# Optimization experiments

Measured on AMD Instinct MI355X. Metric: run time of the kernel, lower is better.

The kernel has to match this reference:

```python
import jax, jax.numpy as jnp
from jax import lax
import numpy as np

EPS = 1e-3  # Keras BatchNormalization default epsilon

def cond_conv(x, experts, rw, rb):
    # x: [B,H,W,Cin]; experts: [E,kh,kw,Cin,Cout]
    pooled = jnp.mean(x, axis=(1, 2))                       # [B,Cin]
    route = jax.nn.sigmoid(pooled @ rw + rb)                # [B,E]
    kernels = jnp.einsum('be,ehwio->bhwio', route, experts) # per-example kernel
    def conv1(xi, ki):
        return lax.conv_general_dilated(
            xi[None], ki, window_strides=(1, 1), padding='SAME',
            dimension_numbers=('NHWC', 'HWIO', 'NHWC'))[0]
    return jax.vmap(conv1)(x, kernels)

def bn_inf(x, gamma, beta, mean, var):
    inv = gamma * lax.rsqrt(var + EPS)
    return x * inv + (beta - mean * inv)

def maxpool2(x):
    return lax.reduce_window(x, -jnp.inf, lax.max,
                             (1, 2, 2, 1), (1, 2, 2, 1), 'SAME')

def se_block(x, w1, w2):
    s = jnp.mean(x, axis=(1, 2))          # [B,C]
    s = jax.nn.relu(s @ w1)
    s = jax.nn.sigmoid(s @ w2)
    return x * s[:, None, None, :]

def setup_inputs() -> dict:
    key = jax.random.key(0)
    ks = jax.random.split(key, 12)
    d = {
        'x': jax.random.normal(ks[0], (64, 128, 128, 6), jnp.float32),
        'experts1': jax.random.normal(ks[1], (3, 3, 3, 6, 32), jnp.float32) * 0.1,
        'route1_w': jax.random.normal(ks[2], (6, 3), jnp.float32) * 0.1,
        'route1_b': jnp.zeros((3,), jnp.float32),
        'bn1_gamma': jnp.ones((32,), jnp.float32), 'bn1_beta': jnp.zeros((32,), jnp.float32),
        'bn1_mean': jnp.zeros((32,), jnp.float32), 'bn1_var': jnp.ones((32,), jnp.float32),
        'se1_w1': jax.random.normal(ks[3], (32, 2), jnp.float32) * 0.1,
        'se1_w2': jax.random.normal(ks[4], (2, 32), jnp.float32) * 0.1,
        'experts2': jax.random.normal(ks[5], (3, 3, 3, 32, 64), jnp.float32) * 0.05,
        'route2_w': jax.random.normal(ks[6], (32, 3), jnp.float32) * 0.1,
        'route2_b': jnp.zeros((3,), jnp.float32),
        'bn2_gamma': jnp.ones((64,), jnp.float32), 'bn2_beta': jnp.zeros((64,), jnp.float32),
        'bn2_mean': jnp.zeros((64,), jnp.float32), 'bn2_var': jnp.ones((64,), jnp.float32),
        'se2_w1': jax.random.normal(ks[7], (64, 4), jnp.float32) * 0.1,
        'se2_w2': jax.random.normal(ks[8], (4, 64), jnp.float32) * 0.1,
        'experts3': jax.random.normal(ks[9], (3, 3, 3, 64, 128), jnp.float32) * 0.05,
        'route3_w': jax.random.normal(ks[10], (64, 3), jnp.float32) * 0.1,
        'route3_b': jnp.zeros((3,), jnp.float32),
        'bn3_gamma': jnp.ones((128,), jnp.float32), 'bn3_beta': jnp.zeros((128,), jnp.float32),
        'bn3_mean': jnp.zeros((128,), jnp.float32), 'bn3_var': jnp.ones((128,), jnp.float32),
    }
    return d

def reference(x, experts1, route1_w, route1_b, bn1_gamma, bn1_beta, bn1_mean, bn1_var,
              se1_w1, se1_w2, experts2, route2_w, route2_b, bn2_gamma, bn2_beta,
              bn2_mean, bn2_var, se2_w1, se2_w2, experts3, route3_w, route3_b,
              bn3_gamma, bn3_beta, bn3_mean, bn3_var):
    h = cond_conv(x, experts1, route1_w, route1_b)
    h = jax.nn.relu(bn_inf(h, bn1_gamma, bn1_beta, bn1_mean, bn1_var))
    h = maxpool2(h)                       # [B,64,64,32]
    h = se_block(h, se1_w1, se1_w2)
    h = cond_conv(h, experts2, route2_w, route2_b)
    h = jax.nn.relu(bn_inf(h, bn2_gamma, bn2_beta, bn2_mean, bn2_var))
    h = maxpool2(h)                       # [B,32,32,64]
    h = se_block(h, se2_w1, se2_w2)
    h = cond_conv(h, experts3, route3_w, route3_b)
    h = bn_inf(h, bn3_gamma, bn3_beta, bn3_mean, bn3_var)
    return jnp.mean(h, axis=(1, 2))       # [B,128]
```

## Files before the change

kernel.cpp:

```cpp
#include <hip/hip_runtime.h>

#define EPSBN 1e-3f

typedef unsigned short ushort_t;
typedef __attribute__((ext_vector_type(8))) short bf8;
typedef __attribute__((ext_vector_type(4))) float f4;

__device__ __forceinline__ float sigmoidf_(float z) {
  return 1.0f / (1.0f + expf(-z));
}

__device__ __forceinline__ ushort_t f2bf(float x) {
  union { float f; unsigned u; } v; v.f = x;
  unsigned r = (v.u + 0x7fffu + ((v.u >> 16) & 1u)) >> 16;
  return (ushort_t)r;
}

__global__ void k_mean_x(const float* __restrict__ x, float* __restrict__ part) {
  const int b = blockIdx.x >> 2;
  const int q = blockIdx.x & 3;
  const int tid = threadIdx.x;
  float acc[6] = {0.f, 0.f, 0.f, 0.f, 0.f, 0.f};
  const float* xb = x + (size_t)b * 98304 + (size_t)q * 24576;
  for (int p = 0; p < 4; ++p) {
    const float* base = xb + (size_t)p * 6144 + (size_t)tid * 24;
#pragma unroll
    for (int k = 0; k < 6; ++k) {
      const float4 v = *(const float4*)(base + k * 4);
      acc[(4 * k + 0) % 6] += v.x;
      acc[(4 * k + 1) % 6] += v.y;
      acc[(4 * k + 2) % 6] += v.z;
      acc[(4 * k + 3) % 6] += v.w;
    }
  }
#pragma unroll
  for (int c = 0; c < 6; ++c)
    for (int off = 32; off > 0; off >>= 1) acc[c] += __shfl_down(acc[c], off, 64);
  __shared__ float red[4][6];
  const int lane = tid & 63, w = tid >> 6;
  if (lane == 0) {
#pragma unroll
    for (int c = 0; c < 6; ++c) red[w][c] = acc[c];
  }
  __syncthreads();
  if (tid < 6) {
    part[blockIdx.x * 6 + tid] = red[0][tid] + red[1][tid] + red[2][tid] + red[3][tid];
  }
}

__global__ __launch_bounds__(256)
void k_conv1(const float* __restrict__ x, const float* __restrict__ meanx_part,
             const float* __restrict__ experts1,
             const float* __restrict__ rw, const float* __restrict__ rbias,
             const float* __restrict__ gamma, const float* __restrict__ beta,
             const float* __restrict__ bnmean, const float* __restrict__ bnvar,
             ushort_t* __restrict__ p1b, float* __restrict__ part_m1) {
  const int bid = blockIdx.x;
  const int b = bid >> 3;
  const int tyi = (bid >> 1) & 3;
  const int txi = bid & 1;
  __shared__ __align__(16) ushort_t patch[34 * 68 * 8];
  __shared__ float route_s[3];
  __shared__ float mred[4][32];
  const int tid = threadIdx.x;
  const float* xb = x + (size_t)b * (128 * 128 * 6);

  if (tid < 3) {
    float z = rbias[tid];
    for (int c = 0; c < 6; ++c) {
      const float s = meanx_part[(b * 4 + 0) * 6 + c] + meanx_part[(b * 4 + 1) * 6 + c] +
                      meanx_part[(b * 4 + 2) * 6 + c] + meanx_part[(b * 4 + 3) * 6 + c];
      z += (s * (1.0f / 16384.0f)) * rw[c * 3 + tid];
    }
    route_s[tid] = sigmoidf_(z);
  }

  for (int v = tid; v < 34 * 68; v += 256) {
    const int ry = v / 68, p = v - ry * 68;
    const int gy = tyi * 32 - 1 + ry, gx = txi * 64 - 1 + p;
    uint4 u = make_uint4(0u, 0u, 0u, 0u);
    if (((unsigned)gy < 128u) && ((unsigned)gx < 128u)) {
      const float* s = xb + ((size_t)(gy * 128 + gx)) * 6;
      const float2 a0 = *(const float2*)s;
      const float2 a1 = *(const float2*)(s + 2);
      const float2 a2 = *(const float2*)(s + 4);
      u.x = (unsigned)f2bf(a0.x) | ((unsigned)f2bf(a0.y) << 16);
      u.y = (unsigned)f2bf(a1.x) | ((unsigned)f2bf(a1.y) << 16);
      u.z = (unsigned)f2bf(a2.x) | ((unsigned)f2bf(a2.y) << 16);
      u.w = 0u;
    }
    *(uint4*)(patch + (size_t)v * 8) = u;
  }
  __syncthreads();

  const int w = tid >> 6;
  const int lane = tid & 63;
  const int lx = lane & 15, lg = lane >> 4;

  const float r0 = route_s[0], r1 = route_s[1], r2 = route_s[2];
  const int co0 = lx, co1 = 16 + lx;
  const float inv0 = gamma[co0] * rsqrtf(bnvar[co0] + EPSBN);
  const float bias0 = beta[co0] - bnmean[co0] * inv0;
  const float inv1 = gamma[co1] * rsqrtf(bnvar[co1] + EPSBN);
  const float bias1 = beta[co1] - bnmean[co1] * inv1;

  bf8 Bf[3][2];
#pragma unroll
  for (int ky = 0; ky < 3; ++ky) {
#pragma unroll
    for (int nt = 0; nt < 2; ++nt) {
      const int co = nt * 16 + lx;
      const float inv = nt ? inv1 : inv0;
#pragma unroll
      for (int j = 0; j < 8; ++j) {
        float val = 0.f;
        if (j < 6 && lg < 3) {
          const int idx = ((ky * 3 + lg) * 6 + j) * 32 + co;
          val = (r0 * experts1[idx] + r1 * experts1[1728 + idx] +
                 r2 * experts1[3456 + idx]) * inv;
        }
        Bf[ky][nt][j] = (short)f2bf(val);
      }
    }
  }

  float msum0 = 0.f, msum1 = 0.f;

#pragma unroll
  for (int xt = 0; xt < 4; ++xt) {
    bf8 Af[10];
#pragma unroll
    for (int r = 0; r < 10; ++r)
      Af[r] = *(const bf8*)(patch + ((size_t)(w * 8 + r) * 68 + xt * 16 + lx + lg) * 8);
#pragma unroll
    for (int rp = 0; rp < 4; ++rp) {
      const int prow = tyi * 16 + w * 4 + rp;
      f4 acc0[2], acc1[2];
#pragma unroll
      for (int nt = 0; nt < 2; ++nt) {
        acc0[nt] = (f4){0.f, 0.f, 0.f, 0.f};
        acc1[nt] = (f4){0.f, 0.f, 0.f, 0.f};
      }
#pragma unroll
      for (int ky = 0; ky < 3; ++ky) {
#pragma unroll
        for (int nt = 0; nt < 2; ++nt) {
          acc0[nt] = __builtin_amdgcn_mfma_f32_16x16x32_bf16(Af[rp * 2 + ky], Bf[ky][nt], acc0[nt], 0, 0, 0);
          acc1[nt] = __builtin_amdgcn_mfma_f32_16x16x32_bf16(Af[rp * 2 + ky + 1], Bf[ky][nt], acc1[nt], 0, 0, 0);
        }
      }
#pragma unroll
      for (int nt = 0; nt < 2; ++nt) {
        const float bias = nt ? bias1 : bias0;
        const int co = nt * 16 + lx;
#pragma unroll
        for (int q = 0; q < 2; ++q) {
          const float m0 = fmaxf(acc0[nt][2 * q] + bias, 0.f);
          const float m1 = fmaxf(acc0[nt][2 * q + 1] + bias, 0.f);
          const float m2 = fmaxf(acc1[nt][2 * q] + bias, 0.f);
          const float m3 = fmaxf(acc1[nt][2 * q + 1] + bias, 0.f);
          const float mx = fmaxf(fmaxf(m0, m1), fmaxf(m2, m3));
          if (nt) msum1 += mx; else msum0 += mx;
          const int pcol = txi * 32 + xt * 8 + lg * 2 + q;
          p1b[(((size_t)b * 64 + prow) * 64 + pcol) * 32 + co] = f2bf(mx);
        }
      }
    }
  }

  msum0 += __shfl_xor(msum0, 16, 64);
  msum0 += __shfl_xor(msum0, 32, 64);
  msum1 += __shfl_xor(msum1, 16, 64);
  msum1 += __shfl_xor(msum1, 32, 64);
  if (lg == 0) {
    mred[w][lx] = msum0;
    mred[w][16 + lx] = msum1;
  }
  __syncthreads();
  if (tid < 32) {
    part_m1[(size_t)bid * 32 + tid] =
        mred[0][tid] + mred[1][tid] + mred[2][tid] + mred[3][tid];
  }
}

__global__ void k_buildk2(const float* __restrict__ part_m1,
                          const float* __restrict__ experts2,
                          const float* __restrict__ rw, const float* __restrict__ rb,
                          const float* __restrict__ w1, const float* __restrict__ w2,
                          const float* __restrict__ gamma, const float* __restrict__ var,
                          ushort_t* __restrict__ k2pb) {
  const int b = blockIdx.x / 3;
  const int seg = blockIdx.x - b * 3;
  const int tid = threadIdx.x;
  __shared__ float m1[32], h[2], s1[32], route[3];
  if (tid < 32) {
    float s = 0.f;
#pragma unroll
    for (int k = 0; k < 8; ++k) s += part_m1[(size_t)(b * 8 + k) * 32 + tid];
    m1[tid] = s * (1.0f / 4096.0f);
  }
  __syncthreads();
  if (tid < 2) {
    float z = 0.f;
    for (int c = 0; c < 32; ++c) z += m1[c] * w1[c * 2 + tid];
    h[tid] = fmaxf(z, 0.f);
  }
  __syncthreads();
  if (tid < 32) s1[tid] = sigmoidf_(h[0] * w2[tid] + h[1] * w2[32 + tid]);
  __syncthreads();
  if (tid < 3) {
    float z = rb[tid];
    for (int c = 0; c < 32; ++c) z += m1[c] * s1[c] * rw[c * 3 + tid];
    route[tid] = sigmoidf_(z);
  }
  __syncthreads();
  const float r0 = route[0], r1 = route[1], r2 = route[2];
  const int t_lo = seg * 6144, t_hi = t_lo + 6144;
  for (int t = t_lo + tid; t < t_hi; t += 256) {
    const int co = t & 63;
    const int ci = (t >> 6) & 31;
    const int tap = t >> 11;
    const float inv = gamma[co] * rsqrtf(var[co] + EPSBN);
    const float v = r0 * experts2[t] + r1 * experts2[18432 + t] + r2 * experts2[2 * 18432 + t];
    k2pb[(size_t)b * 18432 + ((size_t)tap * 64 + co) * 32 + ci] = f2bf(v * s1[ci] * inv);
  }
}

__global__ __launch_bounds__(256)
void k_conv2(const ushort_t* __restrict__ p1b, const ushort_t* __restrict__ k2pb,
             const float* __restrict__ gamma, const float* __restrict__ beta,
             const float* __restrict__ bnmean, const float* __restrict__ bnvar,
             float* __restrict__ part_s3) {
  const int bi = blockIdx.x;
  const int b = bi >> 5;
  const int tile = (bi >> 1) & 15;
  const int cog = bi & 1;
  const int ty = tile >> 2, tx = tile & 3;
  __shared__ __align__(16) short smem[24480];
  short* As = smem;
  short* Bs = smem + 12960;
  const int tid = threadIdx.x;

  const ushort_t* pb = p1b + (size_t)b * 131072;
  for (int v = tid; v < 1296; v += 256) {
    const int cell = v >> 2, part = v & 3;
    const int ly = cell / 18, lx2 = cell - ly * 18;
    const int gy = ty * 16 - 1 + ly, gx = tx * 16 - 1 + lx2;
    uint4 d = make_uint4(0u, 0u, 0u, 0u);
    if (((unsigned)gy < 64u) && ((unsigned)gx < 64u))
      d = *(const uint4*)(pb + (((size_t)gy << 6) + gx) * 32 + part * 8);
    *(uint4*)(As + (ly * 18 + lx2) * 40 + part * 8) = d;
  }
  for (int v = tid; v < 1152; v += 256) {
    const int r = v >> 2, part = v & 3;
    const int t = r >> 5, n = r & 31;
    const uint4 d = *(const uint4*)(k2pb + (size_t)b * 18432 +
                                    ((size_t)(t * 64 + cog * 32 + n)) * 32 + part * 8);
    *(uint4*)(Bs + r * 40 + part * 8) = d;
  }
  __syncthreads();

  const int w = tid >> 6;
  const int lane = tid & 63;
  const int lx = lane & 15, lg = lane >> 4;

  f4 acc[4][2];
#pragma unroll
  for (int mt = 0; mt < 4; ++mt)
#pragma unroll
    for (int nt = 0; nt < 2; ++nt)
      acc[mt][nt] = (f4){0.f, 0.f, 0.f, 0.f};

#pragma unroll
  for (int kx = 0; kx < 3; ++kx) {
    bf8 Af[6];
#pragma unroll
    for (int r = 0; r < 6; ++r)
      Af[r] = *(const bf8*)(As + ((4 * w + r) * 18 + lx + kx) * 40 + (lg << 3));
#pragma unroll
    for (int ky = 0; ky < 3; ++ky) {
      const int t = ky * 3 + kx;
      const bf8 Bf0 = *(const bf8*)(Bs + ((t << 5) + lx) * 40 + (lg << 3));
      const bf8 Bf1 = *(const bf8*)(Bs + ((t << 5) + 16 + lx) * 40 + (lg << 3));
#pragma unroll
      for (int mt = 0; mt < 4; ++mt) {
        acc[mt][0] = __builtin_amdgcn_mfma_f32_16x16x32_bf16(Af[ky + mt], Bf0, acc[mt][0], 0, 0, 0);
        acc[mt][1] = __builtin_amdgcn_mfma_f32_16x16x32_bf16(Af[ky + mt], Bf1, acc[mt][1], 0, 0, 0);
      }
    }
  }

  float inv[2], bias[2];
#pragma unroll
  for (int nt = 0; nt < 2; ++nt) {
    const int co = cog * 32 + nt * 16 + lx;
    inv[nt] = gamma[co] * rsqrtf(bnvar[co] + EPSBN);
    bias[nt] = beta[co] - bnmean[co] * inv[nt];
  }
  float agg[2][9];
#pragma unroll
  for (int nt = 0; nt < 2; ++nt)
#pragma unroll
    for (int a = 0; a < 9; ++a) agg[nt][a] = 0.f;

#pragma unroll
  for (int half = 0; half < 2; ++half) {
    const int prow = ty * 8 + 2 * w + half;
    const bool rT = (prow == 0), rB = (prow == 31);
#pragma unroll
    for (int q = 0; q < 2; ++q) {
      const int pcol = tx * 8 + 2 * lg + q;
      const bool cL = (pcol == 0), cR = (pcol == 31);
#pragma unroll
      for (int nt = 0; nt < 2; ++nt) {
        const float m0 = fmaxf(acc[2 * half][nt][2 * q] + bias[nt], 0.f);
        const float m1 = fmaxf(acc[2 * half][nt][2 * q + 1] + bias[nt], 0.f);
        const float m2 = fmaxf(acc[2 * half + 1][nt][2 * q] + bias[nt], 0.f);
        const float m3 = fmaxf(acc[2 * half + 1][nt][2 * q + 1] + bias[nt], 0.f);
        const float mx = fmaxf(fmaxf(m0, m1), fmaxf(m2, m3));
        agg[nt][0] += mx;
        if (rT) agg[nt][1] += mx;
        if (rB) agg[nt][2] += mx;
        if (cL) agg[nt][3] += mx;
        if (cR) agg[nt][4] += mx;
        if (rT && cL) agg[nt][5] += mx;
        if (rT && cR) agg[nt][6] += mx;
        if (rB && cL) agg[nt][7] += mx;
        if (rB && cR) agg[nt][8] += mx;
      }
    }
  }

#pragma unroll
  for (int nt = 0; nt < 2; ++nt)
#pragma unroll
    for (int a = 0; a < 9; ++a) {
      float v = agg[nt][a];
      v += __shfl_xor(v, 16, 64);
      v += __shfl_xor(v, 32, 64);
      agg[nt][a] = v;
    }
  __syncthreads();
  float* sred = (float*)smem;
  if (lg == 0) {
#pragma unroll
    for (int nt = 0; nt < 2; ++nt)
#pragma unroll
      for (int a = 0; a < 9; ++a)
        sred[((w * 2 + nt) * 16 + lx) * 9 + a] = agg[nt][a];
  }
  __syncthreads();
  for (int v = tid; v < 288; v += 256) {
    const int a = v >> 5;
    const int colocal = v & 31;
    const int nt = colocal >> 4, lxx = colocal & 15;
    float s = 0.f;
#pragma unroll
    for (int ww = 0; ww < 4; ++ww) s += sred[((ww * 2 + nt) * 16 + lxx) * 9 + a];
    part_s3[(size_t)bi * 288 + v] = s;
  }
}

__global__ __launch_bounds__(512)
void k_final(const float* __restrict__ part_s3, const float* __restrict__ experts3,
             const float* __restrict__ rw, const float* __restrict__ rb,
             const float* __restrict__ w1, const float* __restrict__ w2,
             const float* __restrict__ gamma, const float* __restrict__ beta,
             const float* __restrict__ bnmean, const float* __restrict__ bnvar,
             float* __restrict__ out) {
  const int b = blockIdx.x;
  const int tid = threadIdx.x;
  __shared__ float AG[9][64], Sp[9][64], m2[64], h[4], s2[64], route[3], redf[4][128];

  for (int v = tid; v < 576; v += 512) {
    const int a = v >> 6, ci = v & 63;
    const int cg = ci >> 5, colocal = ci & 31;
    float s = 0.f;
#pragma unroll
    for (int tile = 0; tile < 16; ++tile)
      s += part_s3[(size_t)((b * 16 + tile) * 2 + cg) * 288 + a * 32 + colocal];
    AG[a][ci] = s;
  }
  __syncthreads();
  if (tid < 64) m2[tid] = AG[0][tid] * (1.0f / 1024.0f);
  __syncthreads();
  if (tid < 4) {
    float z = 0.f;
    for (int c = 0; c < 64; ++c) z += m2[c] * w1[c * 4 + tid];
    h[tid] = fmaxf(z, 0.f);
  }
  __syncthreads();
  if (tid < 64) {
    float z = 0.f;
#pragma unroll
    for (int j = 0; j < 4; ++j) z += h[j] * w2[j * 64 + tid];
    s2[tid] = sigmoidf_(z);
  }
  __syncthreads();
  if (tid < 3) {
    float z = rb[tid];
    for (int c = 0; c < 64; ++c) z += m2[c] * s2[c] * rw[c * 3 + tid];
    route[tid] = sigmoidf_(z);
  }
  __syncthreads();
  for (int v = tid; v < 576; v += 512) {
    const int tap = v >> 6, ci = v & 63;
    const int ky = tap / 3, kx = tap - 3 * ky;
    const float T = AG[0][ci];
    const float A = (ky == 0) ? AG[2][ci] : ((ky == 2) ? AG[1][ci] : 0.f);
    const float B = (kx == 0) ? AG[4][ci] : ((kx == 2) ? AG[3][ci] : 0.f);
    float AB = 0.f;
    if (ky == 0 && kx == 0) AB = AG[8][ci];
    else if (ky == 0 && kx == 2) AB = AG[7][ci];
    else if (ky == 2 && kx == 0) AB = AG[6][ci];
    else if (ky == 2 && kx == 2) AB = AG[5][ci];
    Sp[tap][ci] = (T - A - B + AB) * s2[ci];
  }
  __syncthreads();

  const int co = tid & 127;
  const int quarter = tid >> 7;
  const int tap_lo = (quarter == 0) ? 0 : (2 * quarter + 1);
  const int tap_hi = tap_lo + ((quarter == 0) ? 3 : 2);
  float acc = 0.f;
#pragma unroll
  for (int e = 0; e < 3; ++e) {
    float m = 0.f;
    for (int tap = tap_lo; tap < tap_hi; ++tap) {
      const float* E = experts3 + ((size_t)(e * 9 + tap) * 64) * 128 + co;
#pragma unroll 16
      for (int ci = 0; ci < 64; ++ci) m = fmaf(E[(size_t)ci * 128], Sp[tap][ci], m);
    }
    acc += route[e] * m;
  }
  redf[quarter][co] = acc;
  __syncthreads();
  if (tid < 128) {
    const float total = redf[0][tid] + redf[1][tid] + redf[2][tid] + redf[3][tid];
    const float inv = gamma[tid] * rsqrtf(bnvar[tid] + EPSBN);
    out[(size_t)b * 128 + tid] = total * (1.0f / 1024.0f) * inv + (beta[tid] - bnmean[tid] * inv);
  }
}

extern "C" void kernel_launch(void* const* d_in, const int* in_sizes, int n_in,
                              void* d_out, int out_size, void* d_ws, size_t ws_size,
                              hipStream_t stream) {
  const float* x        = (const float*)d_in[0];
  const float* experts1 = (const float*)d_in[1];
  const float* rw1      = (const float*)d_in[2];
  const float* rb1      = (const float*)d_in[3];
  const float* g1  = (const float*)d_in[4];
  const float* be1 = (const float*)d_in[5];
  const float* mu1 = (const float*)d_in[6];
  const float* va1 = (const float*)d_in[7];
  const float* sw1a = (const float*)d_in[8];
  const float* sw1b = (const float*)d_in[9];
  const float* experts2 = (const float*)d_in[10];
  const float* rw2 = (const float*)d_in[11];
  const float* rb2 = (const float*)d_in[12];
  const float* g2  = (const float*)d_in[13];
  const float* be2 = (const float*)d_in[14];
  const float* mu2 = (const float*)d_in[15];
  const float* va2 = (const float*)d_in[16];
  const float* sw2a = (const float*)d_in[17];
  const float* sw2b = (const float*)d_in[18];
  const float* experts3 = (const float*)d_in[19];
  const float* rw3 = (const float*)d_in[20];
  const float* rb3 = (const float*)d_in[21];
  const float* g3  = (const float*)d_in[22];
  const float* be3 = (const float*)d_in[23];
  const float* mu3 = (const float*)d_in[24];
  const float* va3 = (const float*)d_in[25];
  float* out = (float*)d_out;
  float* ws = (float*)d_ws;

  float* meanx_part = ws;
  float* part_m1    = ws + 1536;
  ushort_t* k2pb    = (ushort_t*)(ws + 17920);
  float* part_s3    = ws + 607744;
  ushort_t* p1b     = (ushort_t*)(ws + 1197568);

  hipLaunchKernelGGL(k_mean_x, dim3(256), dim3(256), 0, stream, x, meanx_part);
  hipLaunchKernelGGL(k_conv1, dim3(512), dim3(256), 0, stream,
                     x, meanx_part, experts1, rw1, rb1, g1, be1, mu1, va1, p1b, part_m1);
  hipLaunchKernelGGL(k_buildk2, dim3(192), dim3(256), 0, stream,
                     part_m1, experts2, rw2, rb2, sw1a, sw1b, g2, va2, k2pb);
  hipLaunchKernelGGL(k_conv2, dim3(2048), dim3(256), 0, stream,
                     p1b, k2pb, g2, be2, mu2, va2, part_s3);
  hipLaunchKernelGGL(k_final, dim3(64), dim3(512), 0, stream,
                     part_s3, experts3, rw3, rb3, sw2a, sw2b, g3, be3, mu3, va3, out);
}
```

Before: 187.9 us.

## Fuse kernel building and final reduction into conv2 via atomics and last-block tail

Removes the separate k_buildk2 and k_final launches. Each conv2 block now computes routing and builds its own bf16 kernel slice in shared memory. Per-tile statistics are accumulated into a global buffer with atomics, and a per-batch done counter lets the last finishing block run the final SE, routing and expert-3 reduction. This saves two launches and the global round-trips for k2pb and part_s3. In exchange, the expert-2 mix is recomputed redundantly in every block, atomics are added, and the tail work is serialized on one block per batch.

```diff
diff --git a/kernel.cpp b/kernel.cpp
--- a/kernel.cpp
+++ b/kernel.cpp
@@ -16,10 +16,14 @@
   return (ushort_t)r;
 }
 
-__global__ void k_mean_x(const float* __restrict__ x, float* __restrict__ part) {
+__global__ void k_mean_x(const float* __restrict__ x, float* __restrict__ part,
+                         float* __restrict__ S_agg, unsigned* __restrict__ done) {
   const int b = blockIdx.x >> 2;
   const int q = blockIdx.x & 3;
   const int tid = threadIdx.x;
+  if (tid < 144) S_agg[(size_t)b * 576 + q * 144 + tid] = 0.0f;
+  if (q == 0 && tid == 0) done[b] = 0u;
+
   float acc[6] = {0.f, 0.f, 0.f, 0.f, 0.f, 0.f};
   const float* xb = x + (size_t)b * 98304 + (size_t)q * 24576;
   for (int p = 0; p < 4; ++p) {
@@ -125,7 +129,6 @@
   }
 
   float msum0 = 0.f, msum1 = 0.f;
-
 #pragma unroll
   for (int xt = 0; xt < 4; ++xt) {
     bf8 Af[10];
@@ -183,80 +186,80 @@
   }
 }
 
-__global__ void k_buildk2(const float* __restrict__ part_m1,
-                          const float* __restrict__ experts2,
-                          const float* __restrict__ rw, const float* __restrict__ rb,
-                          const float* __restrict__ w1, const float* __restrict__ w2,
-                          const float* __restrict__ gamma, const float* __restrict__ var,
-                          ushort_t* __restrict__ k2pb) {
-  const int b = blockIdx.x / 3;
-  const int seg = blockIdx.x - b * 3;
-  const int tid = threadIdx.x;
-  __shared__ float m1[32], h[2], s1[32], route[3];
-  if (tid < 32) {
-    float s = 0.f;
-#pragma unroll
-    for (int k = 0; k < 8; ++k) s += part_m1[(size_t)(b * 8 + k) * 32 + tid];
-    m1[tid] = s * (1.0f / 4096.0f);
-  }
-  __syncthreads();
-  if (tid < 2) {
-    float z = 0.f;
-    for (int c = 0; c < 32; ++c) z += m1[c] * w1[c * 2 + tid];
-    h[tid] = fmaxf(z, 0.f);
-  }
-  __syncthreads();
-  if (tid < 32) s1[tid] = sigmoidf_(h[0] * w2[tid] + h[1] * w2[32 + tid]);
-  __syncthreads();
-  if (tid < 3) {
-    float z = rb[tid];
-    for (int c = 0; c < 32; ++c) z += m1[c] * s1[c] * rw[c * 3 + tid];
-    route[tid] = sigmoidf_(z);
-  }
-  __syncthreads();
-  const float r0 = route[0], r1 = route[1], r2 = route[2];
-  const int t_lo = seg * 6144, t_hi = t_lo + 6144;
-  for (int t = t_lo + tid; t < t_hi; t += 256) {
-    const int co = t & 63;
-    const int ci = (t >> 6) & 31;
-    const int tap = t >> 11;
-    const float inv = gamma[co] * rsqrtf(var[co] + EPSBN);
-    const float v = r0 * experts2[t] + r1 * experts2[18432 + t] + r2 * experts2[2 * 18432 + t];
-    k2pb[(size_t)b * 18432 + ((size_t)tap * 64 + co) * 32 + ci] = f2bf(v * s1[ci] * inv);
-  }
-}
-
 __global__ __launch_bounds__(256)
-void k_conv2(const ushort_t* __restrict__ p1b, const ushort_t* __restrict__ k2pb,
-             const float* __restrict__ gamma, const float* __restrict__ beta,
-             const float* __restrict__ bnmean, const float* __restrict__ bnvar,
-             float* __restrict__ part_s3) {
+void k_conv2f(const ushort_t* __restrict__ p1b, const float* __restrict__ part_m1,
+              const float* __restrict__ experts2,
+              const float* __restrict__ rw2, const float* __restrict__ rb2,
+              const float* __restrict__ sw1a, const float* __restrict__ sw1b,
+              const float* __restrict__ g2, const float* __restrict__ be2,
+              const float* __restrict__ mu2, const float* __restrict__ va2,
+              const float* __restrict__ experts3,
+              const float* __restrict__ rw3, const float* __restrict__ rb3,
+              const float* __restrict__ sw2a, const float* __restrict__ sw2b,
+              const float* __restrict__ g3, const float* __restrict__ be3,
+              const float* __restrict__ mu3, const float* __restrict__ va3,
+              float* __restrict__ S_agg, unsigned* __restrict__ done,
+              float* __restrict__ out) {
   const int bi = blockIdx.x;
   const int b = bi >> 5;
-  const int tile = (bi >> 1) & 15;
-  const int cog = bi & 1;
-  const int ty = tile >> 2, tx = tile & 3;
-  __shared__ __align__(16) short smem[24480];
-  short* As = smem;
-  short* Bs = smem + 12960;
+  const int ti = bi & 31;
+  const int tile = ti >> 1, cog = ti & 1;
+  const int ty = tile >> 2, tx2 = tile & 3;
+  __shared__ __align__(16) unsigned char smem[53568];
+  __shared__ int is_last;
+  short* As = (short*)smem;
+  short* Bs = As + 12960;
+  float* aux = (float*)(smem + 48960);
   const int tid = threadIdx.x;
 
   const ushort_t* pb = p1b + (size_t)b * 131072;
   for (int v = tid; v < 1296; v += 256) {
     const int cell = v >> 2, part = v & 3;
     const int ly = cell / 18, lx2 = cell - ly * 18;
-    const int gy = ty * 16 - 1 + ly, gx = tx * 16 - 1 + lx2;
+    const int gy = ty * 16 - 1 + ly, gx = tx2 * 16 - 1 + lx2;
     uint4 d = make_uint4(0u, 0u, 0u, 0u);
     if (((unsigned)gy < 64u) && ((unsigned)gx < 64u))
       d = *(const uint4*)(pb + (((size_t)gy << 6) + gx) * 32 + part * 8);
     *(uint4*)(As + (ly * 18 + lx2) * 40 + part * 8) = d;
   }
-  for (int v = tid; v < 1152; v += 256) {
-    const int r = v >> 2, part = v & 3;
-    const int t = r >> 5, n = r & 31;
-    const uint4 d = *(const uint4*)(k2pb + (size_t)b * 18432 +
-                                    ((size_t)(t * 64 + cog * 32 + n)) * 32 + part * 8);
-    *(uint4*)(Bs + r * 40 + part * 8) = d;
+
+  float* m1 = aux;
+  float* h = aux + 32;
+  float* s1 = aux + 36;
+  float* route = aux + 68;
+  if (tid < 32) {
+    float s = 0.f;
+#pragma unroll
+    for (int k = 0; k < 8; ++k) s += part_m1[(size_t)(b * 8 + k) * 32 + tid];
+    m1[tid] = s * (1.0f / 4096.0f);
+  }
+  __syncthreads();
+  if (tid < 2) {
+    float z = 0.f;
+    for (int c = 0; c < 32; ++c) z += m1[c] * sw1a[c * 2 + tid];
+    h[tid] = fmaxf(z, 0.f);
+  }
+  __syncthreads();
+  if (tid < 32) s1[tid] = sigmoidf_(h[0] * sw1b[tid] + h[1] * sw1b[32 + tid]);
+  __syncthreads();
+  if (tid < 3) {
+    float z = rb2[tid];
+    for (int c = 0; c < 32; ++c) z += m1[c] * s1[c] * rw2[c * 3 + tid];
+    route[tid] = sigmoidf_(z);
+  }
+  __syncthreads();
+
+  const float r0 = route[0], r1 = route[1], r2 = route[2];
+  const int n_l = tid & 31;
+  const int co_g = cog * 32 + n_l;
+  const float inv2c = g2[co_g] * rsqrtf(va2[co_g] + EPSBN);
+  for (int j = 0; j < 36; ++j) {
+    const int idx = j * 256 + tid;
+    const int ci = (idx >> 5) & 31;
+    const int tap = idx >> 10;
+    const int t = (tap * 32 + ci) * 64 + co_g;
+    const float v = r0 * experts2[t] + r1 * experts2[18432 + t] + r2 * experts2[36864 + t];
+    Bs[(tap * 32 + n_l) * 40 + ci] = (short)f2bf(v * s1[ci] * inv2c);
   }
   __syncthreads();
 
@@ -294,8 +297,8 @@
 #pragma unroll
   for (int nt = 0; nt < 2; ++nt) {
     const int co = cog * 32 + nt * 16 + lx;
-    inv[nt] = gamma[co] * rsqrtf(bnvar[co] + EPSBN);
-    bias[nt] = beta[co] - bnmean[co] * inv[nt];
+    inv[nt] = g2[co] * rsqrtf(va2[co] + EPSBN);
+    bias[nt] = be2[co] - mu2[co] * inv[nt];
   }
   float agg[2][9];
 #pragma unroll
@@ -309,7 +312,7 @@
     const bool rT = (prow == 0), rB = (prow == 31);
 #pragma unroll
     for (int q = 0; q < 2; ++q) {
-      const int pcol = tx * 8 + 2 * lg + q;
+      const int pcol = tx2 * 8 + 2 * lg + q;
       const bool cL = (pcol == 0), cR = (pcol == 31);
 #pragma unroll
       for (int nt = 0; nt < 2; ++nt) {
@@ -340,8 +343,7 @@
       v += __shfl_xor(v, 32, 64);
       agg[nt][a] = v;
     }
-  __syncthreads();
-  float* sred = (float*)smem;
+  float* sred = aux;
   if (lg == 0) {
 #pragma unroll
     for (int nt = 0; nt < 2; ++nt)
@@ -357,88 +359,84 @@
     float s = 0.f;
 #pragma unroll
     for (int ww = 0; ww < 4; ++ww) s += sred[((ww * 2 + nt) * 16 + lxx) * 9 + a];
-    part_s3[(size_t)bi * 288 + v] = s;
-  }
-}
-
-__global__ __launch_bounds__(512)
-void k_final(const float* __restrict__ part_s3, const float* __restrict__ experts3,
-             const float* __restrict__ rw, const float* __restrict__ rb,
-             const float* __restrict__ w1, const float* __restrict__ w2,
-             const float* __restrict__ gamma, const float* __restrict__ beta,
-             const float* __restrict__ bnmean, const float* __restrict__ bnvar,
-             float* __restrict__ out) {
-  const int b = blockIdx.x;
-  const int tid = threadIdx.x;
-  __shared__ float AG[9][64], Sp[9][64], m2[64], h[4], s2[64], route[3], redf[4][128];
-
-  for (int v = tid; v < 576; v += 512) {
-    const int a = v >> 6, ci = v & 63;
-    const int cg = ci >> 5, colocal = ci & 31;
-    float s = 0.f;
-#pragma unroll
-    for (int tile = 0; tile < 16; ++tile)
-      s += part_s3[(size_t)((b * 16 + tile) * 2 + cg) * 288 + a * 32 + colocal];
-    AG[a][ci] = s;
-  }
-  __syncthreads();
-  if (tid < 64) m2[tid] = AG[0][tid] * (1.0f / 1024.0f);
+    atomicAdd(&S_agg[(size_t)b * 576 + a * 64 + cog * 32 + colocal], s);
+  }
+
+  __syncthreads();
+  if (tid == 0) {
+    const unsigned old = atomicAdd(&done[b], 1u);
+    is_last = (old == 31u) ? 1 : 0;
+  }
+  __syncthreads();
+  if (!is_last) return;
+
+  float* AG = (float*)smem;
+  float* Sp = AG + 576;
+  float* m2 = Sp + 576;
+  float* hh = m2 + 64;
+  float* s2 = hh + 4;
+  float* rt = s2 + 64;
+  float* redf = rt + 4;
+  for (int v = tid; v < 576; v += 256)
+    AG[v] = atomicAdd(&S_agg[(size_t)b * 576 + v], 0.0f);
+  __syncthreads();
+  if (tid < 64) m2[tid] = AG[tid] * (1.0f / 1024.0f);
   __syncthreads();
   if (tid < 4) {
     float z = 0.f;
-    for (int c = 0; c < 64; ++c) z += m2[c] * w1[c * 4 + tid];
-    h[tid] = fmaxf(z, 0.f);
+    for (int c = 0; c < 64; ++c) z += m2[c] * sw2a[c * 4 + tid];
+    hh[tid] = fmaxf(z, 0.f);
   }
   __syncthreads();
   if (tid < 64) {
     float z = 0.f;
 #pragma unroll
-    for (int j = 0; j < 4; ++j) z += h[j] * w2[j * 64 + tid];
+    for (int j = 0; j < 4; ++j) z += hh[j] * sw2b[j * 64 + tid];
     s2[tid] = sigmoidf_(z);
   }
   __syncthreads();
   if (tid < 3) {
-    float z = rb[tid];
-    for (int c = 0; c < 64; ++c) z += m2[c] * s2[c] * rw[c * 3 + tid];
-    route[tid] = sigmoidf_(z);
-  }
-  __syncthreads();
-  for (int v = tid; v < 576; v += 512) {
+    float z = rb3[tid];
+    for (int c = 0; c < 64; ++c) z += m2[c] * s2[c] * rw3[c * 3 + tid];
+    rt[tid] = sigmoidf_(z);
+  }
+  __syncthreads();
+  for (int v = tid; v < 576; v += 256) {
     const int tap = v >> 6, ci = v & 63;
     const int ky = tap / 3, kx = tap - 3 * ky;
-    const float T = AG[0][ci];
-    const float A = (ky == 0) ? AG[2][ci] : ((ky == 2) ? AG[1][ci] : 0.f);
-    const float B = (kx == 0) ? AG[4][ci] : ((kx == 2) ? AG[3][ci] : 0.f);
+    const float T = AG[ci];
+    const float A = (ky == 0) ? AG[2 * 64 + ci] : ((ky == 2) ? AG[1 * 64 + ci] : 0.f);
+    const float B = (kx == 0) ? AG[4 * 64 + ci] : ((kx == 2) ? AG[3 * 64 + ci] : 0.f);
     float AB = 0.f;
-    if (ky == 0 && kx == 0) AB = AG[8][ci];
-    else if (ky == 0 && kx == 2) AB = AG[7][ci];
-    else if (ky == 2 && kx == 0) AB = AG[6][ci];
-    else if (ky == 2 && kx == 2) AB = AG[5][ci];
-    Sp[tap][ci] = (T - A - B + AB) * s2[ci];
+    if (ky == 0 && kx == 0) AB = AG[8 * 64 + ci];
+    else if (ky == 0 && kx == 2) AB = AG[7 * 64 + ci];
+    else if (ky == 2 && kx == 0) AB = AG[6 * 64 + ci];
+    else if (ky == 2 && kx == 2) AB = AG[5 * 64 + ci];
+    Sp[tap * 64 + ci] = (T - A - B + AB) * s2[ci];
   }
   __syncthreads();
 
   const int co = tid & 127;
-  const int quarter = tid >> 7;
-  const int tap_lo = (quarter == 0) ? 0 : (2 * quarter + 1);
-  const int tap_hi = tap_lo + ((quarter == 0) ? 3 : 2);
-  float acc = 0.f;
+  const int hf = tid >> 7;
+  const int tap_lo = hf ? 5 : 0;
+  const int tap_hi = hf ? 9 : 5;
+  float acc2 = 0.f;
 #pragma unroll
   for (int e = 0; e < 3; ++e) {
     float m = 0.f;
     for (int tap = tap_lo; tap < tap_hi; ++tap) {
       const float* E = experts3 + ((size_t)(e * 9 + tap) * 64) * 128 + co;
 #pragma unroll 16
-      for (int ci = 0; ci < 64; ++ci) m = fmaf(E[(size_t)ci * 128], Sp[tap][ci], m);
-    }
-    acc += route[e] * m;
-  }
-  redf[quarter][co] = acc;
+      for (int ci = 0; ci < 64; ++ci) m = fmaf(E[(size_t)ci * 128], Sp[tap * 64 + ci], m);
+    }
+    acc2 += rt[e] * m;
+  }
+  redf[hf * 128 + co] = acc2;
   __syncthreads();
   if (tid < 128) {
-    const float total = redf[0][tid] + redf[1][tid] + redf[2][tid] + redf[3][tid];
-    const float inv = gamma[tid] * rsqrtf(bnvar[tid] + EPSBN);
-    out[(size_t)b * 128 + tid] = total * (1.0f / 1024.0f) * inv + (beta[tid] - bnmean[tid] * inv);
+    const float total = redf[tid] + redf[128 + tid];
+    const float invf = g3[tid] * rsqrtf(va3[tid] + EPSBN);
+    out[(size_t)b * 128 + tid] = total * (1.0f / 1024.0f) * invf + (be3[tid] - mu3[tid] * invf);
   }
 }
 
@@ -476,17 +474,15 @@
 
   float* meanx_part = ws;
   float* part_m1    = ws + 1536;
-  ushort_t* k2pb    = (ushort_t*)(ws + 17920);
-  float* part_s3    = ws + 607744;
-  ushort_t* p1b     = (ushort_t*)(ws + 1197568);
-
-  hipLaunchKernelGGL(k_mean_x, dim3(256), dim3(256), 0, stream, x, meanx_part);
+  float* S_agg      = ws + 17920;
+  unsigned* done    = (unsigned*)(ws + 54784);
+  ushort_t* p1b     = (ushort_t*)(ws + 54848);
+
+  hipLaunchKernelGGL(k_mean_x, dim3(256), dim3(256), 0, stream, x, meanx_part, S_agg, done);
   hipLaunchKernelGGL(k_conv1, dim3(512), dim3(256), 0, stream,
                      x, meanx_part, experts1, rw1, rb1, g1, be1, mu1, va1, p1b, part_m1);
-  hipLaunchKernelGGL(k_buildk2, dim3(192), dim3(256), 0, stream,
-                     part_m1, experts2, rw2, rb2, sw1a, sw1b, g2, va2, k2pb);
-  hipLaunchKernelGGL(k_conv2, dim3(2048), dim3(256), 0, stream,
-                     p1b, k2pb, g2, be2, mu2, va2, part_s3);
-  hipLaunchKernelGGL(k_final, dim3(64), dim3(512), 0, stream,
-                     part_s3, experts3, rw3, rb3, sw2a, sw2b, g3, be3, mu3, va3, out);
-}
+  hipLaunchKernelGGL(k_conv2f, dim3(2048), dim3(256), 0, stream,
+                     p1b, part_m1, experts2, rw2, rb2, sw1a, sw1b, g2, be2, mu2, va2,
+                     experts3, rw3, rb3, sw2a, sw2b, g3, be3, mu3, va3,
+                     S_agg, done, out);
+}
```

Result: slower. 214.7 us (+14.3%).

## Process all 64 output channels per conv2 block to reuse the input patch

Applied to the files above, without the earlier changes.

Each conv2 block now computes all 64 output channels for its spatial tile instead of splitting the channels across two blocks. The kernel weights are loaded in two halves into the same shared buffer, with a barrier between them, while the input patch is loaded once. This halves the grid size and the redundant patch loads and shrinks the partial-sum layout that k_final reads. The cost is twice the accumulator registers per thread, which may lower occupancy, an extra barrier, and fewer blocks to spread across the CUs.

```diff
diff --git a/kernel.cpp b/kernel.cpp
--- a/kernel.cpp
+++ b/kernel.cpp
@@ -125,7 +125,6 @@
   }
 
   float msum0 = 0.f, msum1 = 0.f;
-
 #pragma unroll
   for (int xt = 0; xt < 4; ++xt) {
     bf8 Af[10];
@@ -232,10 +231,9 @@
              const float* __restrict__ bnmean, const float* __restrict__ bnvar,
              float* __restrict__ part_s3) {
   const int bi = blockIdx.x;
-  const int b = bi >> 5;
-  const int tile = (bi >> 1) & 15;
-  const int cog = bi & 1;
-  const int ty = tile >> 2, tx = tile & 3;
+  const int b = bi >> 4;
+  const int tile = bi & 15;
+  const int ty = tile >> 2, tx2 = tile & 3;
   __shared__ __align__(16) short smem[24480];
   short* As = smem;
   short* Bs = smem + 12960;
@@ -245,61 +243,65 @@
   for (int v = tid; v < 1296; v += 256) {
     const int cell = v >> 2, part = v & 3;
     const int ly = cell / 18, lx2 = cell - ly * 18;
-    const int gy = ty * 16 - 1 + ly, gx = tx * 16 - 1 + lx2;
+    const int gy = ty * 16 - 1 + ly, gx = tx2 * 16 - 1 + lx2;
     uint4 d = make_uint4(0u, 0u, 0u, 0u);
     if (((unsigned)gy < 64u) && ((unsigned)gx < 64u))
       d = *(const uint4*)(pb + (((size_t)gy << 6) + gx) * 32 + part * 8);
     *(uint4*)(As + (ly * 18 + lx2) * 40 + part * 8) = d;
   }
-  for (int v = tid; v < 1152; v += 256) {
-    const int r = v >> 2, part = v & 3;
-    const int t = r >> 5, n = r & 31;
-    const uint4 d = *(const uint4*)(k2pb + (size_t)b * 18432 +
-                                    ((size_t)(t * 64 + cog * 32 + n)) * 32 + part * 8);
-    *(uint4*)(Bs + r * 40 + part * 8) = d;
-  }
-  __syncthreads();
 
   const int w = tid >> 6;
   const int lane = tid & 63;
   const int lx = lane & 15, lg = lane >> 4;
 
-  f4 acc[4][2];
+  f4 acc[4][4];
 #pragma unroll
   for (int mt = 0; mt < 4; ++mt)
 #pragma unroll
-    for (int nt = 0; nt < 2; ++nt)
+    for (int nt = 0; nt < 4; ++nt)
       acc[mt][nt] = (f4){0.f, 0.f, 0.f, 0.f};
 
-#pragma unroll
-  for (int kx = 0; kx < 3; ++kx) {
-    bf8 Af[6];
-#pragma unroll
-    for (int r = 0; r < 6; ++r)
-      Af[r] = *(const bf8*)(As + ((4 * w + r) * 18 + lx + kx) * 40 + (lg << 3));
-#pragma unroll
-    for (int ky = 0; ky < 3; ++ky) {
-      const int t = ky * 3 + kx;
-      const bf8 Bf0 = *(const bf8*)(Bs + ((t << 5) + lx) * 40 + (lg << 3));
-      const bf8 Bf1 = *(const bf8*)(Bs + ((t << 5) + 16 + lx) * 40 + (lg << 3));
-#pragma unroll
-      for (int mt = 0; mt < 4; ++mt) {
-        acc[mt][0] = __builtin_amdgcn_mfma_f32_16x16x32_bf16(Af[ky + mt], Bf0, acc[mt][0], 0, 0, 0);
-        acc[mt][1] = __builtin_amdgcn_mfma_f32_16x16x32_bf16(Af[ky + mt], Bf1, acc[mt][1], 0, 0, 0);
-      }
-    }
-  }
-
-  float inv[2], bias[2];
-#pragma unroll
-  for (int nt = 0; nt < 2; ++nt) {
-    const int co = cog * 32 + nt * 16 + lx;
+  for (int hb = 0; hb < 2; ++hb) {
+    if (hb) __syncthreads();
+    for (int v = tid; v < 1152; v += 256) {
+      const int r = v >> 2, part = v & 3;
+      const int t = r >> 5, n = r & 31;
+      const uint4 d = *(const uint4*)(k2pb + (size_t)b * 18432 +
+                                      ((size_t)(t * 64 + hb * 32 + n)) * 32 + part * 8);
+      *(uint4*)(Bs + r * 40 + part * 8) = d;
+    }
+    __syncthreads();
+
+#pragma unroll
+    for (int kx = 0; kx < 3; ++kx) {
+      bf8 Af[6];
+#pragma unroll
+      for (int r = 0; r < 6; ++r)
+        Af[r] = *(const bf8*)(As + ((4 * w + r) * 18 + lx + kx) * 40 + (lg << 3));
+#pragma unroll
+      for (int ky = 0; ky < 3; ++ky) {
+        const int t = ky * 3 + kx;
+        const bf8 Bf0 = *(const bf8*)(Bs + ((t << 5) + lx) * 40 + (lg << 3));
+        const bf8 Bf1 = *(const bf8*)(Bs + ((t << 5) + 16 + lx) * 40 + (lg << 3));
+#pragma unroll
+        for (int mt = 0; mt < 4; ++mt) {
+          acc[mt][hb * 2 + 0] = __builtin_amdgcn_mfma_f32_16x16x32_bf16(Af[ky + mt], Bf0, acc[mt][hb * 2 + 0], 0, 0, 0);
+          acc[mt][hb * 2 + 1] = __builtin_amdgcn_mfma_f32_16x16x32_bf16(Af[ky + mt], Bf1, acc[mt][hb * 2 + 1], 0, 0, 0);
+        }
+      }
+    }
+  }
+
+  float inv[4], bias[4];
+#pragma unroll
+  for (int nt = 0; nt < 4; ++nt) {
+    const int co = nt * 16 + lx;
     inv[nt] = gamma[co] * rsqrtf(bnvar[co] + EPSBN);
     bias[nt] = beta[co] - bnmean[co] * inv[nt];
   }
-  float agg[2][9];
-#pragma unroll
-  for (int nt = 0; nt < 2; ++nt)
+  float agg[4][9];
+#pragma unroll
+  for (int nt = 0; nt < 4; ++nt)
 #pragma unroll
     for (int a = 0; a < 9; ++a) agg[nt][a] = 0.f;
 
@@ -309,10 +311,10 @@
     const bool rT = (prow == 0), rB = (prow == 31);
 #pragma unroll
     for (int q = 0; q < 2; ++q) {
-      const int pcol = tx * 8 + 2 * lg + q;
+      const int pcol = tx2 * 8 + 2 * lg + q;
       const bool cL = (pcol == 0), cR = (pcol == 31);
 #pragma unroll
-      for (int nt = 0; nt < 2; ++nt) {
+      for (int nt = 0; nt < 4; ++nt) {
         const float m0 = fmaxf(acc[2 * half][nt][2 * q] + bias[nt], 0.f);
         const float m1 = fmaxf(acc[2 * half][nt][2 * q + 1] + bias[nt], 0.f);
         const float m2 = fmaxf(acc[2 * half + 1][nt][2 * q] + bias[nt], 0.f);
@@ -332,7 +334,7 @@
   }
 
 #pragma unroll
-  for (int nt = 0; nt < 2; ++nt)
+  for (int nt = 0; nt < 4; ++nt)
 #pragma unroll
     for (int a = 0; a < 9; ++a) {
       float v = agg[nt][a];
@@ -344,20 +346,20 @@
   float* sred = (float*)smem;
   if (lg == 0) {
 #pragma unroll
-    for (int nt = 0; nt < 2; ++nt)
+    for (int nt = 0; nt < 4; ++nt)
 #pragma unroll
       for (int a = 0; a < 9; ++a)
-        sred[((w * 2 + nt) * 16 + lx) * 9 + a] = agg[nt][a];
-  }
-  __syncthreads();
-  for (int v = tid; v < 288; v += 256) {
-    const int a = v >> 5;
-    const int colocal = v & 31;
-    const int nt = colocal >> 4, lxx = colocal & 15;
+        sred[((w * 4 + nt) * 16 + lx) * 9 + a] = agg[nt][a];
+  }
+  __syncthreads();
+  for (int v = tid; v < 576; v += 256) {
+    const int a = v >> 6;
+    const int co = v & 63;
+    const int nt = co >> 4, lxx = co & 15;
     float s = 0.f;
 #pragma unroll
-    for (int ww = 0; ww < 4; ++ww) s += sred[((ww * 2 + nt) * 16 + lxx) * 9 + a];
-    part_s3[(size_t)bi * 288 + v] = s;
+    for (int ww = 0; ww < 4; ++ww) s += sred[((ww * 4 + nt) * 16 + lxx) * 9 + a];
+    part_s3[(size_t)bi * 576 + v] = s;
   }
 }
 
@@ -373,13 +375,11 @@
   __shared__ float AG[9][64], Sp[9][64], m2[64], h[4], s2[64], route[3], redf[4][128];
 
   for (int v = tid; v < 576; v += 512) {
-    const int a = v >> 6, ci = v & 63;
-    const int cg = ci >> 5, colocal = ci & 31;
     float s = 0.f;
 #pragma unroll
     for (int tile = 0; tile < 16; ++tile)
-      s += part_s3[(size_t)((b * 16 + tile) * 2 + cg) * 288 + a * 32 + colocal];
-    AG[a][ci] = s;
+      s += part_s3[(size_t)(b * 16 + tile) * 576 + v];
+    AG[v >> 6][v & 63] = s;
   }
   __syncthreads();
   if (tid < 64) m2[tid] = AG[0][tid] * (1.0f / 1024.0f);
@@ -485,7 +485,7 @@
                      x, meanx_part, experts1, rw1, rb1, g1, be1, mu1, va1, p1b, part_m1);
   hipLaunchKernelGGL(k_buildk2, dim3(192), dim3(256), 0, stream,
                      part_m1, experts2, rw2, rb2, sw1a, sw1b, g2, va2, k2pb);
-  hipLaunchKernelGGL(k_conv2, dim3(2048), dim3(256), 0, stream,
+  hipLaunchKernelGGL(k_conv2, dim3(1024), dim3(256), 0, stream,
                      p1b, k2pb, g2, be2, mu2, va2, part_s3);
   hipLaunchKernelGGL(k_final, dim3(64), dim3(512), 0, stream,
                      part_s3, experts3, rw3, rb3, sw2a, sw2b, g3, be3, mu3, va3, out);
```

Result: no change. 188.8 us (+0.5%).
